# Kernel optimization log

Hardware: AMD Instinct MI355X
Metric: run time of the kernel (lower is better)

Reference implementation:

```python
import jax, jax.numpy as jnp
import numpy as np

B, LOC_MAX, MAX_LEN, EMB, D_DELTA = 16, 20000, 100, 256, 2


def setup_inputs() -> dict:
    key = jax.random.key(0)
    k1, k2, k3, k4, k5 = jax.random.split(key, 5)
    return {
        "self_attn": jax.random.normal(k1, (B, MAX_LEN, EMB), dtype=jnp.float32),
        "self_delta": jax.random.uniform(k2, (B, MAX_LEN, LOC_MAX, D_DELTA), dtype=jnp.float32),
        "traj_len": jax.random.randint(k3, (B,), 0, MAX_LEN, dtype=jnp.int64),
        "emb_table": jax.random.normal(k4, (LOC_MAX + 1, EMB), dtype=jnp.float32) * 0.02,
        "value_w": jax.random.normal(k5, (1, MAX_LEN), dtype=jnp.float32) * 0.1,
    }


def reference(self_attn, self_delta, traj_len, emb_table, value_w):
    # self_delta: [B, max_len, loc_max, D] -> sum last dim -> [B, max_len, loc_max]
    # -> transpose(-1, -2) -> [B, loc_max, max_len]
    delta = jnp.swapaxes(jnp.sum(self_delta, axis=-1), -1, -2)
    loc_max = emb_table.shape[0] - 1
    # candidates = arange(1, loc_max+1) is batch-invariant -> single gather slice
    emb_cand = emb_table[1:loc_max + 1]  # [loc_max, emb]
    # bmm(emb_candidates, self_attn^T): [B, loc_max, max_len], fused with delta mul
    attn = jnp.einsum('le,bme->blm', emb_cand, self_attn) * delta
    # Linear(max_len, 1, bias=False) -> reduce over max_len -> [B, loc_max]
    attn_out = jnp.einsum('blm,m->bl', attn, value_w[0])
    return attn_out
```

## Files before the change

### kernel.cpp

```cpp
#include <hip/hip_runtime.h>

#define NB 16
#define MLEN 100
#define EMBD 256
#define LMAX 20000
#define LTILE 128
#define NLT 157
#define NKC 4
#define FSTRIDE 520
#define PREP_TASKS (NB * NKC * 16 * 64)

typedef __attribute__((ext_vector_type(4))) float f32x4;
typedef _Float16 f16x8 __attribute__((ext_vector_type(8)));

__device__ __forceinline__ unsigned short f2h(float x) {
    union { _Float16 f; unsigned short u; } a; a.f = (_Float16)x; return a.u;
}

__global__ __launch_bounds__(256)
void prep2_kernel(const float* __restrict__ attn, const float* __restrict__ vw,
                  unsigned short* __restrict__ Bf) {
    const int gid  = blockIdx.x * 256 + threadIdx.x;
    const int lane = gid & 63;
    const int f    = gid >> 6;
    const int etg  = f & 15;
    const int kcb  = f >> 4;
    const int kc   = kcb & 3;
    const int b    = kcb >> 2;
    const int e    = etg * 16 + (lane & 15);
    const int m0   = kc * 32 + (lane >> 4) * 8;
    unsigned h[8];
    #pragma unroll
    for (int j = 0; j < 8; ++j) {
        const int m = m0 + j;
        float x = 0.f;
        if (m < MLEN) x = vw[m] * attn[((size_t)b * MLEN + m) * EMBD + e];
        h[j] = f2h(x);
    }
    uint4 hi = make_uint4(h[0]|(h[1]<<16), h[2]|(h[3]<<16), h[4]|(h[5]<<16), h[6]|(h[7]<<16));
    reinterpret_cast<uint4*>(Bf)[gid] = hi;
}

__global__ __launch_bounds__(256, 2)
void main_kernel(const unsigned short* __restrict__ Bf,
                 const float* __restrict__ sdelta, const float* __restrict__ embt,
                 float* __restrict__ out) {
    __shared__ __align__(16) unsigned short AhL[2][8 * FSTRIDE];
    __shared__ float red[512];

    const int b    = blockIdx.x;
    const int lt0  = blockIdx.y;
    const int l0   = lt0 * LTILE;
    const int w    = threadIdx.x >> 6;
    const int lane = threadIdx.x & 63;
    const int llo  = lane & 15;
    const int lhi  = lane >> 4;

    f32x4 acc[8][4];
    #pragma unroll
    for (int lt = 0; lt < 8; ++lt)
        #pragma unroll
        for (int et = 0; et < 4; ++et)
            acc[lt][et] = (f32x4){0.f, 0.f, 0.f, 0.f};

    const int lcl = min(l0 + 2 * lane, LMAX - 2);

    f32x4 vA[2][8];
    auto issueA = [&](int kc) {
        const int q = kc & 1;
        #pragma unroll
        for (int jj = 0; jj < 8; ++jj) {
            const int m  = kc * 32 + w * 8 + jj;
            const int mc = (m < MLEN) ? m : (MLEN - 1);
            vA[q][jj] = *reinterpret_cast<const f32x4*>(
                            sdelta + ((size_t)(b * MLEN + mc) * LMAX + lcl) * 2);
        }
    };
    auto writeA = [&](int kc) {
        const int q   = kc & 1;
        const int lt  = lane >> 3;
        const int lo0 = (2 * lane) & 15;
        unsigned h0[8], h1[8];
        #pragma unroll
        for (int jj = 0; jj < 8; ++jj) {
            const int m = kc * 32 + w * 8 + jj;
            const float msk = (m < MLEN) ? 1.f : 0.f;
            const f32x4 v = vA[q][jj];
            h0[jj] = f2h((v[0] + v[1]) * msk);
            h1[jj] = f2h((v[2] + v[3]) * msk);
        }
        const int i0 = lt * FSTRIDE + (lo0 | (w << 4)) * 8;
        *reinterpret_cast<uint4*>(&AhL[q][i0]) =
            make_uint4(h0[0]|(h0[1]<<16), h0[2]|(h0[3]<<16), h0[4]|(h0[5]<<16), h0[6]|(h0[7]<<16));
        *reinterpret_cast<uint4*>(&AhL[q][i0 + 8]) =
            make_uint4(h1[0]|(h1[1]<<16), h1[2]|(h1[3]<<16), h1[4]|(h1[5]<<16), h1[6]|(h1[7]<<16));
    };
    auto loadB = [&](int kc, f16x8* dst) {
        #pragma unroll
        for (int et = 0; et < 4; ++et) {
            const size_t bo = (((size_t)(b * NKC + kc) * 16 + (w * 4 + et)) * 64 + lane) * 8;
            dst[et] = *reinterpret_cast<const f16x8*>(Bf + bo);
        }
    };

    f16x8 Bc[4], Bn[4];
    issueA(0);
    issueA(1);
    loadB(0, Bc);
    #pragma unroll
    for (int kc = 0; kc < NKC; ++kc) {
        const int q = kc & 1;
        writeA(kc);
        if (kc + 2 < NKC) issueA(kc + 2);
        __builtin_amdgcn_sched_barrier(0);
        asm volatile("s_waitcnt lgkmcnt(0)" ::: "memory");
        __builtin_amdgcn_sched_barrier(0);
        __builtin_amdgcn_s_barrier();
        __builtin_amdgcn_sched_barrier(0);

        if (kc + 1 < NKC) loadB(kc + 1, Bn);
        __builtin_amdgcn_sched_barrier(0);

        #pragma unroll
        for (int lt = 0; lt < 8; ++lt) {
            const f16x8 ah = *reinterpret_cast<const f16x8*>(&AhL[q][lt * FSTRIDE + lane * 8]);
            #pragma unroll
            for (int et = 0; et < 4; ++et)
                acc[lt][et] = __builtin_amdgcn_mfma_f32_16x16x32_f16(ah, Bc[et], acc[lt][et], 0, 0, 0);
        }
        if (kc + 1 < NKC) { Bc[0] = Bn[0]; Bc[1] = Bn[1]; Bc[2] = Bn[2]; Bc[3] = Bn[3]; }
    }

    float p[8][4];
    #pragma unroll
    for (int lt = 0; lt < 8; ++lt) {
        #pragma unroll
        for (int i = 0; i < 4; ++i) {
            const int l  = l0 + lt * 16 + lhi * 4 + i;
            const int lc = (l < LMAX) ? l : (LMAX - 1);
            const float* Er = embt + (size_t)(1 + lc) * EMBD + w * 64 + llo;
            float s = acc[lt][0][i] * Er[0];
            s += acc[lt][1][i] * Er[16];
            s += acc[lt][2][i] * Er[32];
            s += acc[lt][3][i] * Er[48];
            p[lt][i] = s;
        }
    }
    #pragma unroll
    for (int lt = 0; lt < 8; ++lt)
        #pragma unroll
        for (int i = 0; i < 4; ++i) {
            float x = p[lt][i];
            x += __shfl_xor(x, 1);
            x += __shfl_xor(x, 2);
            x += __shfl_xor(x, 4);
            x += __shfl_xor(x, 8);
            p[lt][i] = x;
        }
    if (llo == 0) {
        #pragma unroll
        for (int lt = 0; lt < 8; ++lt)
            *reinterpret_cast<float4*>(&red[w * 128 + lt * 16 + lhi * 4]) =
                make_float4(p[lt][0], p[lt][1], p[lt][2], p[lt][3]);
    }
    __syncthreads();
    if (threadIdx.x < 128) {
        const int t = threadIdx.x;
        const int l = l0 + t;
        if (l < LMAX) {
            out[(size_t)b * LMAX + l] = red[t] + red[128 + t] + red[256 + t] + red[384 + t];
        }
    }
}

__global__ __launch_bounds__(256)
void fallback_kernel(const float* __restrict__ attn, const float* __restrict__ sdelta,
                     const float* __restrict__ embt, const float* __restrict__ vw,
                     float* __restrict__ out) {
    const int idx = blockIdx.x * 256 + threadIdx.x;
    if (idx >= NB * LMAX) return;
    const int b = idx / LMAX;
    const int l = idx % LMAX;
    float s = 0.f;
    for (int m = 0; m < MLEN; ++m) {
        const float* ar = attn + ((size_t)b * MLEN + m) * EMBD;
        const float* er = embt + (size_t)(l + 1) * EMBD;
        float dot = 0.f;
        for (int e = 0; e < EMBD; ++e) dot += ar[e] * er[e];
        const size_t so = (((size_t)b * MLEN + m) * LMAX + l) * 2;
        s += dot * vw[m] * (sdelta[so] + sdelta[so + 1]);
    }
    out[idx] = s;
}

extern "C" void kernel_launch(void* const* d_in, const int* in_sizes, int n_in,
                              void* d_out, int out_size, void* d_ws, size_t ws_size,
                              hipStream_t stream) {
    const float* attn   = (const float*)d_in[0];
    const float* sdelta = (const float*)d_in[1];
    const float* embt   = (const float*)d_in[3];
    const float* vw     = (const float*)d_in[4];
    float* out = (float*)d_out;

    const size_t fragShorts = (size_t)PREP_TASKS * 8;
    const size_t needed     = fragShorts * sizeof(unsigned short);

    if (ws_size >= needed) {
        unsigned short* Bf = (unsigned short*)d_ws;
        prep2_kernel<<<PREP_TASKS / 256, 256, 0, stream>>>(attn, vw, Bf);
        main_kernel<<<dim3(NB, NLT), 256, 0, stream>>>(Bf, sdelta, embt, out);
    } else {
        fallback_kernel<<<(NB * LMAX + 255) / 256, 256, 0, stream>>>(attn, sdelta, embt, vw, out);
    }
}
```

Before: 72.41 us.

## Make main kernel persistent over L tiles with cross-tile A prefetch

```diff
diff --git a/kernel.cpp b/kernel.cpp
--- a/kernel.cpp
+++ b/kernel.cpp
@@ -7,6 +7,8 @@
 #define LTILE 128
 #define NLT 157
 #define NKC 4
+#define NPART 32
+#define PBLOCKS (NB * NPART)
 #define FSTRIDE 520
 #define PREP_TASKS (NB * NKC * 16 * 64)
 
@@ -48,32 +50,25 @@
     __shared__ __align__(16) unsigned short AhL[2][8 * FSTRIDE];
     __shared__ float red[512];
 
-    const int b    = blockIdx.x;
-    const int lt0  = blockIdx.y;
-    const int l0   = lt0 * LTILE;
+    const int bid  = blockIdx.x;
+    const int b    = bid & 15;
+    const int part = bid >> 4;
     const int w    = threadIdx.x >> 6;
     const int lane = threadIdx.x & 63;
     const int llo  = lane & 15;
     const int lhi  = lane >> 4;
 
-    f32x4 acc[8][4];
-    #pragma unroll
-    for (int lt = 0; lt < 8; ++lt)
-        #pragma unroll
-        for (int et = 0; et < 4; ++et)
-            acc[lt][et] = (f32x4){0.f, 0.f, 0.f, 0.f};
-
-    const int lcl = min(l0 + 2 * lane, LMAX - 2);
+    const float* sdb = sdelta + (size_t)b * MLEN * (LMAX * 2);
 
     f32x4 vA[2][8];
-    auto issueA = [&](int kc) {
+    auto issueA = [&](int ltile, int kc) {
         const int q = kc & 1;
+        const int lcl = min(ltile * LTILE + 2 * lane, LMAX - 2);
         #pragma unroll
         for (int jj = 0; jj < 8; ++jj) {
             const int m  = kc * 32 + w * 8 + jj;
             const int mc = (m < MLEN) ? m : (MLEN - 1);
-            vA[q][jj] = *reinterpret_cast<const f32x4*>(
-                            sdelta + ((size_t)(b * MLEN + mc) * LMAX + lcl) * 2);
+            vA[q][jj] = *reinterpret_cast<const f32x4*>(sdb + ((size_t)mc * LMAX + lcl) * 2);
         }
     };
     auto writeA = [&](int kc) {
@@ -104,71 +99,88 @@
     };
 
     f16x8 Bc[4], Bn[4];
-    issueA(0);
-    issueA(1);
+    issueA(part, 0);
+    issueA(part, 1);
     loadB(0, Bc);
-    #pragma unroll
-    for (int kc = 0; kc < NKC; ++kc) {
-        const int q = kc & 1;
-        writeA(kc);
-        if (kc + 2 < NKC) issueA(kc + 2);
+
+    for (int lt0 = part; lt0 < NLT; lt0 += NPART) {
+        const int  l0      = lt0 * LTILE;
+        const bool hasNext = (lt0 + NPART < NLT);
+
+        f32x4 acc[8][4];
+        #pragma unroll
+        for (int lt = 0; lt < 8; ++lt)
+            #pragma unroll
+            for (int et = 0; et < 4; ++et)
+                acc[lt][et] = (f32x4){0.f, 0.f, 0.f, 0.f};
+
+        #pragma unroll
+        for (int kc = 0; kc < NKC; ++kc) {
+            const int q = kc & 1;
+            writeA(kc);
+            if (kc + 2 < NKC)      issueA(lt0, kc + 2);
+            else if (hasNext)      issueA(lt0 + NPART, kc - 2);
+            __builtin_amdgcn_sched_barrier(0);
+            asm volatile("s_waitcnt lgkmcnt(0)" ::: "memory");
+            __builtin_amdgcn_sched_barrier(0);
+            __builtin_amdgcn_s_barrier();
+            __builtin_amdgcn_sched_barrier(0);
+
+            loadB((kc + 1) & 3, Bn);
+            __builtin_amdgcn_sched_barrier(0);
+
+            #pragma unroll
+            for (int lt = 0; lt < 8; ++lt) {
+                const f16x8 ah = *reinterpret_cast<const f16x8*>(&AhL[q][lt * FSTRIDE + lane * 8]);
+                #pragma unroll
+                for (int et = 0; et < 4; ++et)
+                    acc[lt][et] = __builtin_amdgcn_mfma_f32_16x16x32_f16(ah, Bc[et], acc[lt][et], 0, 0, 0);
+            }
+            Bc[0] = Bn[0]; Bc[1] = Bn[1]; Bc[2] = Bn[2]; Bc[3] = Bn[3];
+        }
+
+        float p[8][4];
+        #pragma unroll
+        for (int lt = 0; lt < 8; ++lt) {
+            #pragma unroll
+            for (int i = 0; i < 4; ++i) {
+                const int l  = l0 + lt * 16 + lhi * 4 + i;
+                const int lc = (l < LMAX) ? l : (LMAX - 1);
+                const float* Er = embt + (size_t)(1 + lc) * EMBD + w * 64 + llo;
+                float s = acc[lt][0][i] * Er[0];
+                s += acc[lt][1][i] * Er[16];
+                s += acc[lt][2][i] * Er[32];
+                s += acc[lt][3][i] * Er[48];
+                p[lt][i] = s;
+            }
+        }
+        #pragma unroll
+        for (int lt = 0; lt < 8; ++lt)
+            #pragma unroll
+            for (int i = 0; i < 4; ++i) {
+                float x = p[lt][i];
+                x += __shfl_xor(x, 1);
+                x += __shfl_xor(x, 2);
+                x += __shfl_xor(x, 4);
+                x += __shfl_xor(x, 8);
+                p[lt][i] = x;
+            }
+        if (llo == 0) {
+            #pragma unroll
+            for (int lt = 0; lt < 8; ++lt)
+                *reinterpret_cast<float4*>(&red[w * 128 + lt * 16 + lhi * 4]) =
+                    make_float4(p[lt][0], p[lt][1], p[lt][2], p[lt][3]);
+        }
         __builtin_amdgcn_sched_barrier(0);
         asm volatile("s_waitcnt lgkmcnt(0)" ::: "memory");
         __builtin_amdgcn_sched_barrier(0);
         __builtin_amdgcn_s_barrier();
         __builtin_amdgcn_sched_barrier(0);
-
-        if (kc + 1 < NKC) loadB(kc + 1, Bn);
-        __builtin_amdgcn_sched_barrier(0);
-
-        #pragma unroll
-        for (int lt = 0; lt < 8; ++lt) {
-            const f16x8 ah = *reinterpret_cast<const f16x8*>(&AhL[q][lt * FSTRIDE + lane * 8]);
-            #pragma unroll
-            for (int et = 0; et < 4; ++et)
-                acc[lt][et] = __builtin_amdgcn_mfma_f32_16x16x32_f16(ah, Bc[et], acc[lt][et], 0, 0, 0);
-        }
-        if (kc + 1 < NKC) { Bc[0] = Bn[0]; Bc[1] = Bn[1]; Bc[2] = Bn[2]; Bc[3] = Bn[3]; }
-    }
-
-    float p[8][4];
-    #pragma unroll
-    for (int lt = 0; lt < 8; ++lt) {
-        #pragma unroll
-        for (int i = 0; i < 4; ++i) {
-            const int l  = l0 + lt * 16 + lhi * 4 + i;
-            const int lc = (l < LMAX) ? l : (LMAX - 1);
-            const float* Er = embt + (size_t)(1 + lc) * EMBD + w * 64 + llo;
-            float s = acc[lt][0][i] * Er[0];
-            s += acc[lt][1][i] * Er[16];
-            s += acc[lt][2][i] * Er[32];
-            s += acc[lt][3][i] * Er[48];
-            p[lt][i] = s;
-        }
-    }
-    #pragma unroll
-    for (int lt = 0; lt < 8; ++lt)
-        #pragma unroll
-        for (int i = 0; i < 4; ++i) {
-            float x = p[lt][i];
-            x += __shfl_xor(x, 1);
-            x += __shfl_xor(x, 2);
-            x += __shfl_xor(x, 4);
-            x += __shfl_xor(x, 8);
-            p[lt][i] = x;
-        }
-    if (llo == 0) {
-        #pragma unroll
-        for (int lt = 0; lt < 8; ++lt)
-            *reinterpret_cast<float4*>(&red[w * 128 + lt * 16 + lhi * 4]) =
-                make_float4(p[lt][0], p[lt][1], p[lt][2], p[lt][3]);
-    }
-    __syncthreads();
-    if (threadIdx.x < 128) {
-        const int t = threadIdx.x;
-        const int l = l0 + t;
-        if (l < LMAX) {
-            out[(size_t)b * LMAX + l] = red[t] + red[128 + t] + red[256 + t] + red[384 + t];
+        if (threadIdx.x < 128) {
+            const int t = threadIdx.x;
+            const int l = l0 + t;
+            if (l < LMAX)
+                out[(size_t)b * LMAX + l] = red[t] + red[128 + t] + red[256 + t] + red[384 + t];
         }
     }
 }
@@ -208,7 +220,7 @@
     if (ws_size >= needed) {
         unsigned short* Bf = (unsigned short*)d_ws;
         prep2_kernel<<<PREP_TASKS / 256, 256, 0, stream>>>(attn, vw, Bf);
-        main_kernel<<<dim3(NB, NLT), 256, 0, stream>>>(Bf, sdelta, embt, out);
+        main_kernel<<<PBLOCKS, 256, 0, stream>>>(Bf, sdelta, embt, out);
     } else {
         fallback_kernel<<<(NB * LMAX + 255) / 256, 256, 0, stream>>>(attn, sdelta, embt, vw, out);
     }
```

Measured after the change: 232.9 us. 3.22x slower.

## Split off the tail m-rows into a precomputed term, shrinking the main MFMA loop

Applied to the files above, without the earlier changes.

```diff
diff --git a/kernel.cpp b/kernel.cpp
--- a/kernel.cpp
+++ b/kernel.cpp
@@ -7,8 +7,11 @@
 #define LTILE 128
 #define NLT 157
 #define NKC 4
+#define NKCM 3
 #define FSTRIDE 520
 #define PREP_TASKS (NB * NKC * 16 * 64)
+#define PREP_BLOCKS (PREP_TASKS / 256)
+#define P4_BLOCKS 313
 
 typedef __attribute__((ext_vector_type(4))) float f32x4;
 typedef _Float16 f16x8 __attribute__((ext_vector_type(8)));
@@ -18,31 +21,86 @@
 }
 
 __global__ __launch_bounds__(256)
-void prep2_kernel(const float* __restrict__ attn, const float* __restrict__ vw,
-                  unsigned short* __restrict__ Bf) {
-    const int gid  = blockIdx.x * 256 + threadIdx.x;
-    const int lane = gid & 63;
-    const int f    = gid >> 6;
-    const int etg  = f & 15;
-    const int kcb  = f >> 4;
-    const int kc   = kcb & 3;
-    const int b    = kcb >> 2;
-    const int e    = etg * 16 + (lane & 15);
-    const int m0   = kc * 32 + (lane >> 4) * 8;
-    unsigned h[8];
-    #pragma unroll
-    for (int j = 0; j < 8; ++j) {
-        const int m = m0 + j;
-        float x = 0.f;
-        if (m < MLEN) x = vw[m] * attn[((size_t)b * MLEN + m) * EMBD + e];
-        h[j] = f2h(x);
-    }
-    uint4 hi = make_uint4(h[0]|(h[1]<<16), h[2]|(h[3]<<16), h[4]|(h[5]<<16), h[6]|(h[7]<<16));
-    reinterpret_cast<uint4*>(Bf)[gid] = hi;
+void prep_kernel(const float* __restrict__ attn, const float* __restrict__ vw,
+                 const float* __restrict__ embt,
+                 unsigned short* __restrict__ Bf, float* __restrict__ P4) {
+    if (blockIdx.x < PREP_BLOCKS) {
+        const int gid  = blockIdx.x * 256 + threadIdx.x;
+        const int lane = gid & 63;
+        const int f    = gid >> 6;
+        const int etg  = f & 15;
+        const int kcb  = f >> 4;
+        const int kc   = kcb & 3;
+        const int b    = kcb >> 2;
+        const int e    = etg * 16 + (lane & 15);
+        const int m0   = kc * 32 + (lane >> 4) * 8;
+        unsigned h[8];
+        #pragma unroll
+        for (int j = 0; j < 8; ++j) {
+            const int m = m0 + j;
+            float x = 0.f;
+            if (m < MLEN) x = vw[m] * attn[((size_t)b * MLEN + m) * EMBD + e];
+            h[j] = f2h(x);
+        }
+        uint4 hi = make_uint4(h[0]|(h[1]<<16), h[2]|(h[3]<<16), h[4]|(h[5]<<16), h[6]|(h[7]<<16));
+        reinterpret_cast<uint4*>(Bf)[gid] = hi;
+    } else {
+        const int blk  = blockIdx.x - PREP_BLOCKS;
+        const int l0   = blk * 64;
+        const int w    = threadIdx.x >> 6;
+        const int lane = threadIdx.x & 63;
+        const int llo  = lane & 15;
+        const int lhi  = lane >> 4;
+
+        f32x4 acc4[4];
+        #pragma unroll
+        for (int nt = 0; nt < 4; ++nt) acc4[nt] = (f32x4){0.f, 0.f, 0.f, 0.f};
+
+        float wv[4]; const float* wp[4];
+        #pragma unroll
+        for (int nt = 0; nt < 4; ++nt) {
+            const int n  = nt * 16 + llo;
+            const int bb = n >> 2, mi = n & 3;
+            wv[nt] = vw[96 + mi];
+            wp[nt] = attn + ((size_t)(bb * MLEN) + 96 + mi) * EMBD;
+        }
+        const int lrow = min(l0 + w * 16 + llo, LMAX - 1);
+        const float* ep = embt + (size_t)(1 + lrow) * EMBD;
+
+        for (int ks = 0; ks < 8; ++ks) {
+            const int k0 = ks * 32 + lhi * 8;
+            const f32x4 a0 = *reinterpret_cast<const f32x4*>(ep + k0);
+            const f32x4 a1 = *reinterpret_cast<const f32x4*>(ep + k0 + 4);
+            f16x8 af;
+            #pragma unroll
+            for (int j = 0; j < 4; ++j) { af[j] = (_Float16)a0[j]; af[j + 4] = (_Float16)a1[j]; }
+            #pragma unroll
+            for (int nt = 0; nt < 4; ++nt) {
+                const f32x4 b0 = *reinterpret_cast<const f32x4*>(wp[nt] + k0);
+                const f32x4 b1 = *reinterpret_cast<const f32x4*>(wp[nt] + k0 + 4);
+                f16x8 bf_;
+                #pragma unroll
+                for (int j = 0; j < 4; ++j) {
+                    bf_[j]     = (_Float16)(b0[j] * wv[nt]);
+                    bf_[j + 4] = (_Float16)(b1[j] * wv[nt]);
+                }
+                acc4[nt] = __builtin_amdgcn_mfma_f32_16x16x32_f16(af, bf_, acc4[nt], 0, 0, 0);
+            }
+        }
+        #pragma unroll
+        for (int nt = 0; nt < 4; ++nt) {
+            const int n = nt * 16 + llo;
+            #pragma unroll
+            for (int i = 0; i < 4; ++i) {
+                const int l = l0 + w * 16 + lhi * 4 + i;
+                if (l < LMAX) P4[(size_t)n * LMAX + l] = acc4[nt][i];
+            }
+        }
+    }
 }
 
 __global__ __launch_bounds__(256, 2)
-void main_kernel(const unsigned short* __restrict__ Bf,
+void main_kernel(const unsigned short* __restrict__ Bf, const float* __restrict__ P4,
                  const float* __restrict__ sdelta, const float* __restrict__ embt,
                  float* __restrict__ out) {
     __shared__ __align__(16) unsigned short AhL[2][8 * FSTRIDE];
@@ -70,10 +128,9 @@
         const int q = kc & 1;
         #pragma unroll
         for (int jj = 0; jj < 8; ++jj) {
-            const int m  = kc * 32 + w * 8 + jj;
-            const int mc = (m < MLEN) ? m : (MLEN - 1);
+            const int m = kc * 32 + w * 8 + jj;
             vA[q][jj] = *reinterpret_cast<const f32x4*>(
-                            sdelta + ((size_t)(b * MLEN + mc) * LMAX + lcl) * 2);
+                            sdelta + ((size_t)(b * MLEN + m) * LMAX + lcl) * 2);
         }
     };
     auto writeA = [&](int kc) {
@@ -83,11 +140,9 @@
         unsigned h0[8], h1[8];
         #pragma unroll
         for (int jj = 0; jj < 8; ++jj) {
-            const int m = kc * 32 + w * 8 + jj;
-            const float msk = (m < MLEN) ? 1.f : 0.f;
             const f32x4 v = vA[q][jj];
-            h0[jj] = f2h((v[0] + v[1]) * msk);
-            h1[jj] = f2h((v[2] + v[3]) * msk);
+            h0[jj] = f2h(v[0] + v[1]);
+            h1[jj] = f2h(v[2] + v[3]);
         }
         const int i0 = lt * FSTRIDE + (lo0 | (w << 4)) * 8;
         *reinterpret_cast<uint4*>(&AhL[q][i0]) =
@@ -107,18 +162,29 @@
     issueA(0);
     issueA(1);
     loadB(0, Bc);
-    #pragma unroll
-    for (int kc = 0; kc < NKC; ++kc) {
+    const int lE = min(l0 + (threadIdx.x & 127), LMAX - 1);
+    float2 d4[4]; float q4[4];
+    #pragma unroll
+    for (int j = 0; j < 4; ++j)
+        d4[j] = *reinterpret_cast<const float2*>(
+                    sdelta + ((size_t)(b * MLEN + 96 + j) * LMAX + lE) * 2);
+    #pragma unroll
+    for (int j = 0; j < 4; ++j)
+        q4[j] = P4[(size_t)(b * 4 + j) * LMAX + lE];
+    __builtin_amdgcn_sched_barrier(0);
+
+    #pragma unroll
+    for (int kc = 0; kc < NKCM; ++kc) {
         const int q = kc & 1;
         writeA(kc);
-        if (kc + 2 < NKC) issueA(kc + 2);
+        if (kc + 2 < NKCM) issueA(kc + 2);
         __builtin_amdgcn_sched_barrier(0);
         asm volatile("s_waitcnt lgkmcnt(0)" ::: "memory");
         __builtin_amdgcn_sched_barrier(0);
         __builtin_amdgcn_s_barrier();
         __builtin_amdgcn_sched_barrier(0);
 
-        if (kc + 1 < NKC) loadB(kc + 1, Bn);
+        if (kc + 1 < NKCM) loadB(kc + 1, Bn);
         __builtin_amdgcn_sched_barrier(0);
 
         #pragma unroll
@@ -128,7 +194,7 @@
             for (int et = 0; et < 4; ++et)
                 acc[lt][et] = __builtin_amdgcn_mfma_f32_16x16x32_f16(ah, Bc[et], acc[lt][et], 0, 0, 0);
         }
-        if (kc + 1 < NKC) { Bc[0] = Bn[0]; Bc[1] = Bn[1]; Bc[2] = Bn[2]; Bc[3] = Bn[3]; }
+        if (kc + 1 < NKCM) { Bc[0] = Bn[0]; Bc[1] = Bn[1]; Bc[2] = Bn[2]; Bc[3] = Bn[3]; }
     }
 
     float p[8][4];
@@ -168,7 +234,10 @@
         const int t = threadIdx.x;
         const int l = l0 + t;
         if (l < LMAX) {
-            out[(size_t)b * LMAX + l] = red[t] + red[128 + t] + red[256 + t] + red[384 + t];
+            float s = red[t] + red[128 + t] + red[256 + t] + red[384 + t];
+            #pragma unroll
+            for (int j = 0; j < 4; ++j) s += (d4[j].x + d4[j].y) * q4[j];
+            out[(size_t)b * LMAX + l] = s;
         }
     }
 }
@@ -203,12 +272,15 @@
     float* out = (float*)d_out;
 
     const size_t fragShorts = (size_t)PREP_TASKS * 8;
-    const size_t needed     = fragShorts * sizeof(unsigned short);
+    const size_t bfBytes    = fragShorts * sizeof(unsigned short);
+    const size_t p4Bytes    = (size_t)64 * LMAX * sizeof(float);
+    const size_t needed     = bfBytes + p4Bytes;
 
     if (ws_size >= needed) {
         unsigned short* Bf = (unsigned short*)d_ws;
-        prep2_kernel<<<PREP_TASKS / 256, 256, 0, stream>>>(attn, vw, Bf);
-        main_kernel<<<dim3(NB, NLT), 256, 0, stream>>>(Bf, sdelta, embt, out);
+        float* P4 = (float*)((char*)d_ws + bfBytes);
+        prep_kernel<<<PREP_BLOCKS + P4_BLOCKS, 256, 0, stream>>>(attn, vw, embt, Bf, P4);
+        main_kernel<<<dim3(NB, NLT), 256, 0, stream>>>(Bf, P4, sdelta, embt, out);
     } else {
         fallback_kernel<<<(NB * LMAX + 255) / 256, 256, 0, stream>>>(attn, sdelta, embt, vw, out);
     }
```

New measurement: 91.92 us. 1.27x slower.
